# Performance work log

Measured on AMD Instinct MI355X. Metric: run time of the kernel, lower is better.

## Reference

```python
import jax, jax.numpy as jnp
import numpy as np

B, S, D = 4, 2048, 2048        # batch, seq, input_size (== hidden_size)
H, O = 2048, 2048              # expert hidden, output_size (== D -> no shortcut)
E, K = 8, 2                    # num_experts, top_k
CAP_F = 1.25


def setup_inputs() -> dict:
    key = jax.random.key(0)
    ks = jax.random.split(key, 7)
    scale = 0.02
    return {
        "x": jax.random.normal(ks[0], (B, S, D), jnp.float32),
        "gate_w": jax.random.normal(ks[1], (D, E), jnp.float32) * scale,
        "gate_b": jnp.zeros((E,), jnp.float32),
        "temperature": jnp.ones((1,), jnp.float32) * 0.5,
        "w1": jax.random.normal(ks[2], (E, D, H), jnp.float32) * scale,
        "b1": jnp.zeros((E, H), jnp.float32),
        "w2": jax.random.normal(ks[3], (E, H, O), jnp.float32) * scale,
        "b2": jnp.zeros((E, O), jnp.float32),
    }


def reference(x, gate_w, gate_b, temperature, w1, b1, w2, b2):
    b, s, d = x.shape
    n = b * s
    flat = x.reshape(n, d)

    # --- router (eval path: no noisy gating) ---
    logits = (flat @ gate_w + gate_b) / jnp.abs(temperature)
    probs = jax.nn.softmax(logits.astype(jnp.float32), axis=-1)   # [n, E]
    rw, sel = jax.lax.top_k(probs, K)                              # [n, K]
    rw = rw / rw.sum(axis=-1, keepdims=True)

    capacity = int(CAP_F * n * K / E)  # static
    out = jnp.zeros((n, O), flat.dtype)

    for e in range(E):  # fixed small expert count; data dims stay vectorized
        mask = sel == e                                   # [n, K]
        wm = jnp.where(mask, rw, -1.0).reshape(-1)        # [n*K], sentinel -1
        top_w, top_pos = jax.lax.top_k(wm, capacity)      # capacity-limited by weight
        tok = top_pos // K                                # token indices
        w = jnp.where(top_w > 0.0, top_w, 0.0)[:, None].astype(flat.dtype)
        xin = flat[tok]                                   # [cap, D] gather
        h = jax.nn.relu(xin @ w1[e] + b1[e])              # [cap, H]
        y = h @ w2[e] + b2[e]                             # [cap, O]
        out = out.at[tok].add(y * w)                      # scatter-add combine

    output = (out + flat).reshape(b, s, O)  # shortcut is None since D == O

    # --- load-balance aux loss ---
    avg_prob = probs.mean(axis=0)                         # [E]
    usage = jax.nn.one_hot(sel, E, dtype=jnp.float32).sum(axis=1)  # [n, E]
    avg_usage = usage.mean(axis=0)
    balance = E * jnp.sum(avg_prob * avg_usage)
    imp = probs.sum(axis=0)
    cv = jnp.std(imp, ddof=1) / (jnp.mean(imp) + 1e-10)   # torch.std is unbiased
    aux_loss = balance + 0.01 * cv
    return output, aux_loss
```

## Files before the change

kernel.cpp:

```cpp
#include <hip/hip_runtime.h>
#include <math.h>

#define N_TOK 8192
#define DIM 2048
#define HDIM 2048
#define ODIM 2048
#define NEXP 8
#define CAPACITY 2560

typedef __bf16 bf16x8 __attribute__((ext_vector_type(8)));
typedef float f32x4 __attribute__((ext_vector_type(4)));

__device__ __forceinline__ void async16(const void* g, void* l) {
  __builtin_amdgcn_global_load_lds(
      (const __attribute__((address_space(1))) void*)g,
      (__attribute__((address_space(3))) void*)l, 16, 0, 0);
}

__global__ __launch_bounds__(64) void router_kernel(
    const float* __restrict__ x, const float* __restrict__ gate_w,
    const float* __restrict__ gate_b, const float* __restrict__ temp,
    float* __restrict__ probs, int* __restrict__ sel, float* __restrict__ rwv,
    __bf16* __restrict__ xb) {
  int t = blockIdx.x;
  int lane = threadIdx.x;
  const float* xr = x + (size_t)t * DIM;
  __bf16* xbr = xb + (size_t)t * DIM;
  float part[NEXP];
#pragma unroll
  for (int e = 0; e < NEXP; e++) part[e] = 0.f;
  for (int k = lane; k < DIM; k += 64) {
    float xv = xr[k];
    xbr[k] = (__bf16)xv;
    const float* gw = gate_w + (size_t)k * NEXP;
#pragma unroll
    for (int e = 0; e < NEXP; e++) part[e] += xv * gw[e];
  }
#pragma unroll
  for (int e = 0; e < NEXP; e++) {
    float v = part[e];
#pragma unroll
    for (int off = 32; off > 0; off >>= 1) v += __shfl_down(v, off);
    part[e] = v;
  }
  if (lane == 0) {
    float it = 1.0f / fabsf(temp[0]);
    float lg[NEXP];
    float m = -1e30f;
#pragma unroll
    for (int e = 0; e < NEXP; e++) {
      lg[e] = (part[e] + gate_b[e]) * it;
      m = fmaxf(m, lg[e]);
    }
    float s = 0.f;
    float p[NEXP];
#pragma unroll
    for (int e = 0; e < NEXP; e++) { p[e] = expf(lg[e] - m); s += p[e]; }
    float inv_s = 1.f / s;
#pragma unroll
    for (int e = 0; e < NEXP; e++) { p[e] *= inv_s; probs[(size_t)t * NEXP + e] = p[e]; }
    int e1 = 0;
#pragma unroll
    for (int e = 1; e < NEXP; e++) if (p[e] > p[e1]) e1 = e;
    int e2 = -1;
#pragma unroll
    for (int e = 0; e < NEXP; e++) {
      if (e == e1) continue;
      if (e2 < 0 || p[e] > p[e2]) e2 = e;
    }
    float s2 = p[e1] + p[e2];
    sel[t * 2 + 0] = e1;
    sel[t * 2 + 1] = e2;
    rwv[t * 2 + 0] = p[e1] / s2;
    rwv[t * 2 + 1] = p[e2] / s2;
  }
}

__global__ __launch_bounds__(256) void aux_kernel(
    const float* __restrict__ probs, const int* __restrict__ sel,
    float* __restrict__ aux_out, int* __restrict__ cnt_assign,
    int* __restrict__ list_cnt) {
  int tid = threadIdx.x;
  float lps[NEXP];
  int lc[NEXP];
#pragma unroll
  for (int e = 0; e < NEXP; e++) { lps[e] = 0.f; lc[e] = 0; }
  for (int t = tid; t < N_TOK; t += 256) {
    const float* pr = probs + (size_t)t * NEXP;
#pragma unroll
    for (int e = 0; e < NEXP; e++) lps[e] += pr[e];
  }
  for (int j = tid; j < N_TOK * 2; j += 256) lc[sel[j]]++;
  __shared__ float sps[NEXP][256];
  __shared__ int scs[NEXP][256];
#pragma unroll
  for (int e = 0; e < NEXP; e++) { sps[e][tid] = lps[e]; scs[e][tid] = lc[e]; }
  __syncthreads();
  for (int off = 128; off > 0; off >>= 1) {
    if (tid < off) {
#pragma unroll
      for (int e = 0; e < NEXP; e++) {
        sps[e][tid] += sps[e][tid + off];
        scs[e][tid] += scs[e][tid + off];
      }
    }
    __syncthreads();
  }
  if (tid < NEXP) {
    cnt_assign[tid] = scs[tid][0];
    list_cnt[tid] = 0;
  }
  if (tid == 0) {
    float ps[NEXP];
    int cs[NEXP];
#pragma unroll
    for (int e = 0; e < NEXP; e++) { ps[e] = sps[e][0]; cs[e] = scs[e][0]; }
    float balance = 0.f;
#pragma unroll
    for (int e = 0; e < NEXP; e++)
      balance += (ps[e] / (float)N_TOK) * ((float)cs[e] / (float)N_TOK);
    balance *= (float)NEXP;
    float meanimp = 0.f;
#pragma unroll
    for (int e = 0; e < NEXP; e++) meanimp += ps[e];
    meanimp /= (float)NEXP;
    float var = 0.f;
#pragma unroll
    for (int e = 0; e < NEXP; e++) { float d = ps[e] - meanimp; var += d * d; }
    var /= (float)(NEXP - 1);
    float cv = sqrtf(var) / (meanimp + 1e-10f);
    aux_out[0] = balance + 0.01f * cv;
  }
}

__global__ __launch_bounds__(256) void transpose_cvt_kernel(
    const float* __restrict__ w1, const float* __restrict__ w2,
    ushort* __restrict__ wt_all) {
  int z = blockIdx.z;
  const float* src = (z < 8) ? (w1 + (size_t)z * DIM * HDIM)
                             : (w2 + (size_t)(z - 8) * HDIM * ODIM);
  ushort* dst = wt_all + (size_t)z * 2048 * 2048;
  __shared__ float tile[64][68];
  int tid = threadIdx.x;
  int k0 = blockIdx.x * 64;
  int n0 = blockIdx.y * 64;
  int tr = tid >> 4;
  int tc = (tid & 15) * 4;
#pragma unroll
  for (int i = 0; i < 4; i++) {
    int r = tr + i * 16;
    float4 v = *(const float4*)(src + (size_t)(k0 + r) * 2048 + n0 + tc);
    *(float4*)&tile[r][tc] = v;
  }
  __syncthreads();
#pragma unroll
  for (int i = 0; i < 4; i++) {
    int n = tr + i * 16;
    __bf16 o[4];
#pragma unroll
    for (int j = 0; j < 4; j++) o[j] = (__bf16)tile[tc + j][n];
    *(ushort4*)(dst + (size_t)(n0 + n) * 2048 + k0 + tc) = *(const ushort4*)o;
  }
}

__global__ __launch_bounds__(256) void build_lists(
    const int* __restrict__ sel, const float* __restrict__ rwv,
    const int* __restrict__ cnt_assign, int* __restrict__ list_cnt,
    int* __restrict__ etok, int* __restrict__ pos) {
  int j = blockIdx.x * blockDim.x + threadIdx.x;
  if (j >= N_TOK * 2) return;
  int e = sel[j];
  float w = rwv[j];
  bool keep = true;
  if (cnt_assign[e] > CAPACITY) {
    int rank = 0;
    for (int j2 = 0; j2 < N_TOK * 2; j2++) {
      if (sel[j2] == e) {
        float w2 = rwv[j2];
        if (w2 > w || (w2 == w && j2 < j)) rank++;
      }
    }
    keep = (rank < CAPACITY);
  }
  if (keep) {
    int slot = atomicAdd(&list_cnt[e], 1);
    etok[(size_t)e * CAPACITY + slot] = j >> 1;
    pos[j] = e * CAPACITY + slot;
  } else {
    pos[j] = -1;
  }
}


#define BAR() asm volatile("s_barrier" ::: "memory")
#define VMCNT6() asm volatile("s_waitcnt vmcnt(6)" ::: "memory")

#define STAGE_A(d, h, t)                                                    \
  do {                                                                      \
    int _k0 = ((t) & 31) * 64;                                              \
    async16(gaP[(h) * 2 + 0] + _k0, dstA + (d) * 32768 + (h) * 16384);      \
    async16(gaP[(h) * 2 + 1] + _k0, dstA + (d) * 32768 + (h) * 16384 + 8192); \
  } while (0)

#define STAGE_B(d, h, t)                                                    \
  do {                                                                      \
    int _k0 = ((t) & 31) * 64;                                              \
    async16(gbP[(h) * 2 + 0] + _k0, dstB + (d) * 32768 + (h) * 16384);      \
    async16(gbP[(h) * 2 + 1] + _k0, dstB + (d) * 32768 + (h) * 16384 + 8192); \
  } while (0)

#define LOAD_B(d)                                                           \
  do {                                                                      \
    _Pragma("unroll") for (int nt = 0; nt < 4; nt++) {                      \
      bfr[nt][0] = *(const bf16x8*)(smem + (d) * 32768 + boff + nt * 2048 + kx0); \
      bfr[nt][1] = *(const bf16x8*)(smem + (d) * 32768 + boff + nt * 2048 + kx1); \
    }                                                                       \
  } while (0)

#define LOAD_A(d, q)                                                        \
  do {                                                                      \
    _Pragma("unroll") for (int s = 0; s < 2; s++) {                         \
      af[s][0] = *(const bf16x8*)(smem + (d) * 32768 + ((q) >> 1) * 16384 + \
                                  ((q) & 1) * 8192 + aoff + s * 2048 + kx0); \
      af[s][1] = *(const bf16x8*)(smem + (d) * 32768 + ((q) >> 1) * 16384 + \
                                  ((q) & 1) * 8192 + aoff + s * 2048 + kx1); \
    }                                                                       \
  } while (0)

#define MFMA_PH(q)                                                          \
  do {                                                                      \
    __builtin_amdgcn_s_setprio(1);                                          \
    _Pragma("unroll") for (int s = 0; s < 2; s++)                           \
    _Pragma("unroll") for (int nt = 0; nt < 4; nt++) {                      \
      acc[(q) * 2 + s][nt] = __builtin_amdgcn_mfma_f32_16x16x32_bf16(       \
          af[s][0], bfr[nt][0], acc[(q) * 2 + s][nt], 0, 0, 0);             \
      acc[(q) * 2 + s][nt] = __builtin_amdgcn_mfma_f32_16x16x32_bf16(       \
          af[s][1], bfr[nt][1], acc[(q) * 2 + s][nt], 0, 0, 0);             \
    }                                                                       \
    __builtin_amdgcn_s_setprio(0);                                          \
  } while (0)

template <bool GATHER, bool RELU>
__global__ __launch_bounds__(512, 2) void mfma_ffn_8ph(
    const __bf16* __restrict__ Abase, const __bf16* __restrict__ Wt,
    const float* __restrict__ bias, const int* __restrict__ etok,
    const int* __restrict__ list_cnt, __bf16* __restrict__ Out) {
  __shared__ __align__(16) char smem[131072];

  int id = blockIdx.x;
  int nid = (id & 7) * 80 + (id >> 3);
  int bx = nid % 10;
  int by = (nid / 10) & 7;
  int e = nid / 80;
  int cnt = list_cnt[e];
  int row0 = bx * 256;
  if (row0 >= cnt) return;
  int col0 = by * 256;

  const __bf16* We = Wt + (size_t)e * DIM * DIM;
  const int* etok_e = etok + e * CAPACITY;
  const float* bias_e = bias + (size_t)e * DIM;
  __bf16* OutE = Out + (size_t)e * CAPACITY * DIM;

  int tid = threadIdx.x;
  int rA = tid >> 3;
  int kp = tid & 7;

  const __bf16* gaP[4];
  const __bf16* gbP[4];
#pragma unroll
  for (int h = 0; h < 2; h++) {
#pragma unroll
    for (int g = 0; g < 2; g++) {
      int r = h * 128 + g * 64 + rA;
      int kl = kp ^ (r & 7);
      int arow = row0 + r;
      const __bf16* ap;
      if (GATHER) {
        int tok = (arow < cnt) ? etok_e[arow] : 0;
        ap = Abase + (size_t)tok * DIM;
      } else {
        ap = Abase + (size_t)e * CAPACITY * DIM + (size_t)arow * DIM;
      }
      gaP[h * 2 + g] = ap + kl * 8;
      gbP[h * 2 + g] = We + (size_t)(col0 + r) * DIM + kl * 8;
    }
  }
  char* dstA = smem + tid * 16;
  char* dstB = smem + 65536 + tid * 16;

  int wid = tid >> 6, lane = tid & 63;
  int wm = wid >> 2, wn = wid & 3;
  int lm = lane & 15, lg = lane >> 4;
  int kx0 = ((0 * 4 + lg) ^ (lm & 7)) * 16;
  int kx1 = ((1 * 4 + lg) ^ (lm & 7)) * 16;
  int aoff = (wm * 32 + lm) * 128;
  int boff = 65536 + (wn >> 1) * 16384 + ((wn & 1) * 64 + lm) * 128;

  f32x4 acc[8][4] = {};
  bf16x8 bfr[4][2];
  bf16x8 af[2][2];

  STAGE_B(0, 0, 0); STAGE_B(0, 1, 0); STAGE_A(0, 0, 0); STAGE_A(0, 1, 0);
  STAGE_B(1, 0, 1); STAGE_B(1, 1, 1); STAGE_A(1, 0, 1);
  VMCNT6();
  BAR();

#pragma unroll 1
  for (int j = 0; j < 16; j++) {
    int t1 = 2 * j + 1, t2 = 2 * j + 2, t3 = 2 * j + 3;
    LOAD_B(0); LOAD_A(0, 0); STAGE_A(1, 1, t1);
    BAR(); MFMA_PH(0); BAR();
    LOAD_A(0, 1); STAGE_B(0, 0, t2);
    BAR(); MFMA_PH(1); BAR();
    LOAD_A(0, 2); STAGE_B(0, 1, t2);
    BAR(); MFMA_PH(2); BAR();
    LOAD_A(0, 3); STAGE_A(0, 0, t2);
    VMCNT6();
    BAR(); MFMA_PH(3); BAR();
    LOAD_B(1); LOAD_A(1, 0); STAGE_A(0, 1, t2);
    BAR(); MFMA_PH(0); BAR();
    LOAD_A(1, 1); STAGE_B(1, 0, t3);
    BAR(); MFMA_PH(1); BAR();
    LOAD_A(1, 2); STAGE_B(1, 1, t3);
    BAR(); MFMA_PH(2); BAR();
    LOAD_A(1, 3); STAGE_A(1, 0, t3);
    VMCNT6();
    BAR(); MFMA_PH(3); BAR();
  }

  asm volatile("s_waitcnt vmcnt(0)" ::: "memory");
  __syncthreads();

  float bcol[4];
#pragma unroll
  for (int nt = 0; nt < 4; nt++) bcol[nt] = bias_e[col0 + wn * 64 + nt * 16 + lm];

  __bf16* T = (__bf16*)smem;
#pragma unroll
  for (int p = 0; p < 2; p++) {
    if (p) __syncthreads();
#pragma unroll
    for (int u = 0; u < 4; u++) {
      int am = 4 * p + u;
      int rbase = ((am >> 1) & 1) * 64 + wm * 32 + (am & 1) * 16 + lg * 4;
#pragma unroll
      for (int nt = 0; nt < 4; nt++) {
        int col = wn * 64 + nt * 16 + lm;
#pragma unroll
        for (int reg = 0; reg < 4; reg++) {
          float v = acc[am][nt][reg] + bcol[nt];
          if (RELU) v = fmaxf(v, 0.f);
          T[(rbase + reg) * 268 + col] = (__bf16)v;
        }
      }
    }
    __syncthreads();
    int rr = tid >> 2, s4 = (tid & 3) * 64;
    const __bf16* srcp = T + rr * 268 + s4;
    __bf16* dstp = OutE + (size_t)(row0 + p * 128 + rr) * DIM + col0 + s4;
#pragma unroll
    for (int i = 0; i < 8; i++)
      *(bf16x8*)(dstp + i * 8) = *(const bf16x8*)(srcp + i * 8);
  }
}

__global__ __launch_bounds__(256) void combine_kernel(
    const float* __restrict__ x, const __bf16* __restrict__ ybuf,
    const int* __restrict__ pos, const float* __restrict__ rwv,
    float* __restrict__ out) {
  int t = blockIdx.x;
  int tid = threadIdx.x;
  int c = tid * 8;
  int p0 = pos[t * 2 + 0], p1 = pos[t * 2 + 1];
  float w0 = rwv[t * 2 + 0], w1 = rwv[t * 2 + 1];
  const float* xr = x + (size_t)t * DIM + c;
  float4 v0 = *(const float4*)(xr);
  float4 v1 = *(const float4*)(xr + 4);
  float o[8] = {v0.x, v0.y, v0.z, v0.w, v1.x, v1.y, v1.z, v1.w};
  if (p0 >= 0) {
    bf16x8 y = *(const bf16x8*)(ybuf + (size_t)p0 * ODIM + c);
#pragma unroll
    for (int i = 0; i < 8; i++) o[i] += w0 * (float)y[i];
  }
  if (p1 >= 0) {
    bf16x8 y = *(const bf16x8*)(ybuf + (size_t)p1 * ODIM + c);
#pragma unroll
    for (int i = 0; i < 8; i++) o[i] += w1 * (float)y[i];
  }
  float* orow = out + (size_t)t * ODIM + c;
  *(float4*)(orow) = make_float4(o[0], o[1], o[2], o[3]);
  *(float4*)(orow + 4) = make_float4(o[4], o[5], o[6], o[7]);
}

extern "C" void kernel_launch(void* const* d_in, const int* in_sizes, int n_in,
                              void* d_out, int out_size, void* d_ws, size_t ws_size,
                              hipStream_t stream) {
  const float* x = (const float*)d_in[0];
  const float* gate_w = (const float*)d_in[1];
  const float* gate_b = (const float*)d_in[2];
  const float* temp = (const float*)d_in[3];
  const float* w1 = (const float*)d_in[4];
  const float* b1 = (const float*)d_in[5];
  const float* w2 = (const float*)d_in[6];
  const float* b2 = (const float*)d_in[7];
  float* out = (float*)d_out;

  char* ws = (char*)d_ws;
  size_t off = 0;
  float* probs = (float*)(ws + off); off += (size_t)N_TOK * NEXP * 4;
  int* sel = (int*)(ws + off);       off += (size_t)N_TOK * 2 * 4;
  float* rwv = (float*)(ws + off);   off += (size_t)N_TOK * 2 * 4;
  int* cnt_assign = (int*)(ws + off); off += 64;
  int* list_cnt = (int*)(ws + off);   off += 64;
  int* etok = (int*)(ws + off);      off += (size_t)NEXP * CAPACITY * 4;
  int* pos = (int*)(ws + off);       off += (size_t)N_TOK * 2 * 4;
  off = (off + 255) & ~(size_t)255;
  __bf16* xb = (__bf16*)(ws + off);   off += (size_t)N_TOK * DIM * 2;
  ushort* wt_all = (ushort*)(ws + off); off += (size_t)16 * 2048 * 2048 * 2;
  __bf16* hbuf = (__bf16*)(ws + off); off += (size_t)NEXP * CAPACITY * HDIM * 2;
  __bf16* ybuf = xb;

  router_kernel<<<N_TOK, 64, 0, stream>>>(x, gate_w, gate_b, temp, probs, sel, rwv, xb);
  float* aux_out = out + (size_t)N_TOK * ODIM;
  aux_kernel<<<1, 256, 0, stream>>>(probs, sel, aux_out, cnt_assign, list_cnt);
  dim3 tgrid(32, 32, 16);
  transpose_cvt_kernel<<<tgrid, 256, 0, stream>>>(w1, w2, wt_all);
  build_lists<<<(N_TOK * 2 + 255) / 256, 256, 0, stream>>>(sel, rwv, cnt_assign,
                                                           list_cnt, etok, pos);
  const __bf16* w1t = (const __bf16*)wt_all;
  const __bf16* w2t = (const __bf16*)(wt_all + (size_t)8 * 2048 * 2048);
  mfma_ffn_8ph<true, true><<<640, 512, 0, stream>>>(xb, w1t, b1, etok, list_cnt, hbuf);
  mfma_ffn_8ph<false, false><<<640, 512, 0, stream>>>(hbuf, w2t, b2, etok, list_cnt, ybuf);
  combine_kernel<<<N_TOK, 256, 0, stream>>>(x, ybuf, pos, rwv, out);
}
```

Measured before the change: 829.2 us.

## Use persistent compacted tile map for expert FFN GEMMs

Adds a build_tiles kernel that lists only the non-empty (expert, row-block, col-block) tiles. The two FFN GEMM kernels then run as a persistent grid of 256 blocks that loop over that list, replacing 640 blocks that often exit early. The goal is to avoid idle or early-exiting blocks and balance work across CUs. It costs an extra tiny launch and loses the previous XCD-aware block remapping. The transpose kernel's shared tile padding is also changed from 68 to 65 with scalar stores, which targets bank conflicts.

```diff
diff --git a/kernel.cpp b/kernel.cpp
--- a/kernel.cpp
+++ b/kernel.cpp
@@ -7,6 +7,7 @@
 #define ODIM 2048
 #define NEXP 8
 #define CAPACITY 2560
+#define MAXTILES 640
 
 typedef __bf16 bf16x8 __attribute__((ext_vector_type(8)));
 typedef float f32x4 __attribute__((ext_vector_type(4)));
@@ -140,7 +141,7 @@
   const float* src = (z < 8) ? (w1 + (size_t)z * DIM * HDIM)
                              : (w2 + (size_t)(z - 8) * HDIM * ODIM);
   ushort* dst = wt_all + (size_t)z * 2048 * 2048;
-  __shared__ float tile[64][68];
+  __shared__ float tile[64][65];
   int tid = threadIdx.x;
   int k0 = blockIdx.x * 64;
   int n0 = blockIdx.y * 64;
@@ -150,7 +151,10 @@
   for (int i = 0; i < 4; i++) {
     int r = tr + i * 16;
     float4 v = *(const float4*)(src + (size_t)(k0 + r) * 2048 + n0 + tc);
-    *(float4*)&tile[r][tc] = v;
+    tile[r][tc + 0] = v.x;
+    tile[r][tc + 1] = v.y;
+    tile[r][tc + 2] = v.z;
+    tile[r][tc + 3] = v.w;
   }
   __syncthreads();
 #pragma unroll
@@ -191,6 +195,33 @@
   }
 }
 
+__global__ __launch_bounds__(64) void build_tiles(
+    const int* __restrict__ list_cnt, int* __restrict__ tilemap) {
+  __shared__ int pre[NEXP + 1];
+  int tid = threadIdx.x;
+  if (tid == 0) {
+    int acc = 0;
+    for (int e = 0; e < NEXP; e++) {
+      pre[e] = acc;
+      int c = list_cnt[e];
+      acc += ((c + 255) >> 8) * 8;
+    }
+    pre[NEXP] = acc;
+    tilemap[0] = acc;
+  }
+  __syncthreads();
+  int total = pre[NEXP];
+  for (int e = 0; e < NEXP; e++) {
+    int base = pre[e];
+    int n = pre[e + 1] - base;
+    for (int l = tid; l < n; l += 64) {
+      int bx = l >> 3;
+      int by = l & 7;
+      tilemap[1 + base + l] = (e << 16) | (bx << 8) | by;
+    }
+  }
+}
+
 
 #define BAR() asm volatile("s_barrier" ::: "memory")
 #define VMCNT6() asm volatile("s_waitcnt vmcnt(6)" ::: "memory")
@@ -244,48 +275,15 @@
 __global__ __launch_bounds__(512, 2) void mfma_ffn_8ph(
     const __bf16* __restrict__ Abase, const __bf16* __restrict__ Wt,
     const float* __restrict__ bias, const int* __restrict__ etok,
-    const int* __restrict__ list_cnt, __bf16* __restrict__ Out) {
+    const int* __restrict__ list_cnt, const int* __restrict__ tilemap,
+    __bf16* __restrict__ Out) {
   __shared__ __align__(16) char smem[131072];
 
-  int id = blockIdx.x;
-  int nid = (id & 7) * 80 + (id >> 3);
-  int bx = nid % 10;
-  int by = (nid / 10) & 7;
-  int e = nid / 80;
-  int cnt = list_cnt[e];
-  int row0 = bx * 256;
-  if (row0 >= cnt) return;
-  int col0 = by * 256;
-
-  const __bf16* We = Wt + (size_t)e * DIM * DIM;
-  const int* etok_e = etok + e * CAPACITY;
-  const float* bias_e = bias + (size_t)e * DIM;
-  __bf16* OutE = Out + (size_t)e * CAPACITY * DIM;
+  int Ttiles = tilemap[0];
 
   int tid = threadIdx.x;
   int rA = tid >> 3;
   int kp = tid & 7;
-
-  const __bf16* gaP[4];
-  const __bf16* gbP[4];
-#pragma unroll
-  for (int h = 0; h < 2; h++) {
-#pragma unroll
-    for (int g = 0; g < 2; g++) {
-      int r = h * 128 + g * 64 + rA;
-      int kl = kp ^ (r & 7);
-      int arow = row0 + r;
-      const __bf16* ap;
-      if (GATHER) {
-        int tok = (arow < cnt) ? etok_e[arow] : 0;
-        ap = Abase + (size_t)tok * DIM;
-      } else {
-        ap = Abase + (size_t)e * CAPACITY * DIM + (size_t)arow * DIM;
-      }
-      gaP[h * 2 + g] = ap + kl * 8;
-      gbP[h * 2 + g] = We + (size_t)(col0 + r) * DIM + kl * 8;
-    }
-  }
   char* dstA = smem + tid * 16;
   char* dstB = smem + 65536 + tid * 16;
 
@@ -297,71 +295,109 @@
   int aoff = (wm * 32 + lm) * 128;
   int boff = 65536 + (wn >> 1) * 16384 + ((wn & 1) * 64 + lm) * 128;
 
-  f32x4 acc[8][4] = {};
-  bf16x8 bfr[4][2];
-  bf16x8 af[2][2];
-
-  STAGE_B(0, 0, 0); STAGE_B(0, 1, 0); STAGE_A(0, 0, 0); STAGE_A(0, 1, 0);
-  STAGE_B(1, 0, 1); STAGE_B(1, 1, 1); STAGE_A(1, 0, 1);
-  VMCNT6();
-  BAR();
+  for (int it = blockIdx.x; it < Ttiles; it += 256) {
+    int enc = tilemap[1 + it];
+    int e = enc >> 16;
+    int bx = (enc >> 8) & 255;
+    int by = enc & 255;
+    int cnt = list_cnt[e];
+    int row0 = bx * 256;
+    int col0 = by * 256;
+
+    const __bf16* We = Wt + (size_t)e * DIM * DIM;
+    const int* etok_e = etok + e * CAPACITY;
+    const float* bias_e = bias + (size_t)e * DIM;
+    __bf16* OutE = Out + (size_t)e * CAPACITY * DIM;
+
+    const __bf16* gaP[4];
+    const __bf16* gbP[4];
+#pragma unroll
+    for (int h = 0; h < 2; h++) {
+#pragma unroll
+      for (int g = 0; g < 2; g++) {
+        int r = h * 128 + g * 64 + rA;
+        int kl = kp ^ (r & 7);
+        int arow = row0 + r;
+        const __bf16* ap;
+        if (GATHER) {
+          int tok = (arow < cnt) ? etok_e[arow] : 0;
+          ap = Abase + (size_t)tok * DIM;
+        } else {
+          ap = Abase + (size_t)e * CAPACITY * DIM + (size_t)arow * DIM;
+        }
+        gaP[h * 2 + g] = ap + kl * 8;
+        gbP[h * 2 + g] = We + (size_t)(col0 + r) * DIM + kl * 8;
+      }
+    }
+
+    f32x4 acc[8][4] = {};
+    bf16x8 bfr[4][2];
+    bf16x8 af[2][2];
+
+    STAGE_B(0, 0, 0); STAGE_B(0, 1, 0); STAGE_A(0, 0, 0); STAGE_A(0, 1, 0);
+    STAGE_B(1, 0, 1); STAGE_B(1, 1, 1); STAGE_A(1, 0, 1);
+    VMCNT6();
+    BAR();
 
 #pragma unroll 1
-  for (int j = 0; j < 16; j++) {
-    int t1 = 2 * j + 1, t2 = 2 * j + 2, t3 = 2 * j + 3;
-    LOAD_B(0); LOAD_A(0, 0); STAGE_A(1, 1, t1);
-    BAR(); MFMA_PH(0); BAR();
-    LOAD_A(0, 1); STAGE_B(0, 0, t2);
-    BAR(); MFMA_PH(1); BAR();
-    LOAD_A(0, 2); STAGE_B(0, 1, t2);
-    BAR(); MFMA_PH(2); BAR();
-    LOAD_A(0, 3); STAGE_A(0, 0, t2);
-    VMCNT6();
-    BAR(); MFMA_PH(3); BAR();
-    LOAD_B(1); LOAD_A(1, 0); STAGE_A(0, 1, t2);
-    BAR(); MFMA_PH(0); BAR();
-    LOAD_A(1, 1); STAGE_B(1, 0, t3);
-    BAR(); MFMA_PH(1); BAR();
-    LOAD_A(1, 2); STAGE_B(1, 1, t3);
-    BAR(); MFMA_PH(2); BAR();
-    LOAD_A(1, 3); STAGE_A(1, 0, t3);
-    VMCNT6();
-    BAR(); MFMA_PH(3); BAR();
-  }
-
-  asm volatile("s_waitcnt vmcnt(0)" ::: "memory");
-  __syncthreads();
-
-  float bcol[4];
-#pragma unroll
-  for (int nt = 0; nt < 4; nt++) bcol[nt] = bias_e[col0 + wn * 64 + nt * 16 + lm];
-
-  __bf16* T = (__bf16*)smem;
-#pragma unroll
-  for (int p = 0; p < 2; p++) {
-    if (p) __syncthreads();
-#pragma unroll
-    for (int u = 0; u < 4; u++) {
-      int am = 4 * p + u;
-      int rbase = ((am >> 1) & 1) * 64 + wm * 32 + (am & 1) * 16 + lg * 4;
-#pragma unroll
-      for (int nt = 0; nt < 4; nt++) {
-        int col = wn * 64 + nt * 16 + lm;
-#pragma unroll
-        for (int reg = 0; reg < 4; reg++) {
-          float v = acc[am][nt][reg] + bcol[nt];
-          if (RELU) v = fmaxf(v, 0.f);
-          T[(rbase + reg) * 268 + col] = (__bf16)v;
+    for (int j = 0; j < 16; j++) {
+      int t1 = 2 * j + 1, t2 = 2 * j + 2, t3 = 2 * j + 3;
+      LOAD_B(0); LOAD_A(0, 0); STAGE_A(1, 1, t1);
+      BAR(); MFMA_PH(0); BAR();
+      LOAD_A(0, 1); STAGE_B(0, 0, t2);
+      BAR(); MFMA_PH(1); BAR();
+      LOAD_A(0, 2); STAGE_B(0, 1, t2);
+      BAR(); MFMA_PH(2); BAR();
+      LOAD_A(0, 3); STAGE_A(0, 0, t2);
+      VMCNT6();
+      BAR(); MFMA_PH(3); BAR();
+      LOAD_B(1); LOAD_A(1, 0); STAGE_A(0, 1, t2);
+      BAR(); MFMA_PH(0); BAR();
+      LOAD_A(1, 1); STAGE_B(1, 0, t3);
+      BAR(); MFMA_PH(1); BAR();
+      LOAD_A(1, 2); STAGE_B(1, 1, t3);
+      BAR(); MFMA_PH(2); BAR();
+      LOAD_A(1, 3); STAGE_A(1, 0, t3);
+      VMCNT6();
+      BAR(); MFMA_PH(3); BAR();
+    }
+
+    asm volatile("s_waitcnt vmcnt(0)" ::: "memory");
+    __syncthreads();
+
+    float bcol[4];
+#pragma unroll
+    for (int nt = 0; nt < 4; nt++)
+      bcol[nt] = bias_e[col0 + wn * 64 + nt * 16 + lm];
+
+    __bf16* T = (__bf16*)smem;
+#pragma unroll
+    for (int p = 0; p < 2; p++) {
+      if (p) __syncthreads();
+#pragma unroll
+      for (int u = 0; u < 4; u++) {
+        int am = 4 * p + u;
+        int rbase = ((am >> 1) & 1) * 64 + wm * 32 + (am & 1) * 16 + lg * 4;
+#pragma unroll
+        for (int nt = 0; nt < 4; nt++) {
+          int col = wn * 64 + nt * 16 + lm;
+#pragma unroll
+          for (int reg = 0; reg < 4; reg++) {
+            float v = acc[am][nt][reg] + bcol[nt];
+            if (RELU) v = fmaxf(v, 0.f);
+            T[(rbase + reg) * 268 + col] = (__bf16)v;
+          }
         }
       }
+      __syncthreads();
+      int rr = tid >> 2, s4 = (tid & 3) * 64;
+      const __bf16* srcp = T + rr * 268 + s4;
+      __bf16* dstp = OutE + (size_t)(row0 + p * 128 + rr) * DIM + col0 + s4;
+#pragma unroll
+      for (int i = 0; i < 8; i++)
+        *(bf16x8*)(dstp + i * 8) = *(const bf16x8*)(srcp + i * 8);
     }
     __syncthreads();
-    int rr = tid >> 2, s4 = (tid & 3) * 64;
-    const __bf16* srcp = T + rr * 268 + s4;
-    __bf16* dstp = OutE + (size_t)(row0 + p * 128 + rr) * DIM + col0 + s4;
-#pragma unroll
-    for (int i = 0; i < 8; i++)
-      *(bf16x8*)(dstp + i * 8) = *(const bf16x8*)(srcp + i * 8);
   }
 }
 
@@ -415,6 +451,7 @@
   int* list_cnt = (int*)(ws + off);   off += 64;
   int* etok = (int*)(ws + off);      off += (size_t)NEXP * CAPACITY * 4;
   int* pos = (int*)(ws + off);       off += (size_t)N_TOK * 2 * 4;
+  int* tilemap = (int*)(ws + off);   off += (size_t)(1 + MAXTILES) * 4;
   off = (off + 255) & ~(size_t)255;
   __bf16* xb = (__bf16*)(ws + off);   off += (size_t)N_TOK * DIM * 2;
   ushort* wt_all = (ushort*)(ws + off); off += (size_t)16 * 2048 * 2048 * 2;
@@ -428,9 +465,12 @@
   transpose_cvt_kernel<<<tgrid, 256, 0, stream>>>(w1, w2, wt_all);
   build_lists<<<(N_TOK * 2 + 255) / 256, 256, 0, stream>>>(sel, rwv, cnt_assign,
                                                            list_cnt, etok, pos);
+  build_tiles<<<1, 64, 0, stream>>>(list_cnt, tilemap);
   const __bf16* w1t = (const __bf16*)wt_all;
   const __bf16* w2t = (const __bf16*)(wt_all + (size_t)8 * 2048 * 2048);
-  mfma_ffn_8ph<true, true><<<640, 512, 0, stream>>>(xb, w1t, b1, etok, list_cnt, hbuf);
-  mfma_ffn_8ph<false, false><<<640, 512, 0, stream>>>(hbuf, w2t, b2, etok, list_cnt, ybuf);
+  mfma_ffn_8ph<true, true><<<256, 512, 0, stream>>>(xb, w1t, b1, etok, list_cnt,
+                                                    tilemap, hbuf);
+  mfma_ffn_8ph<false, false><<<256, 512, 0, stream>>>(hbuf, w2t, b2, etok, list_cnt,
+                                                      tilemap, ybuf);
   combine_kernel<<<N_TOK, 256, 0, stream>>>(x, ybuf, pos, rwv, out);
 }
```

Measured after the change: 859.7 us. +3.7%, slower.
